# Performance work log

Hardware: AMD Instinct MI355X
Metric: run time of the kernel (lower is better)

## Reference

```python
import math
import jax, jax.numpy as jnp
import numpy as np

B, S, D_MODEL, H = 2, 2048, 1024, 16
D_HEAD = D_MODEL // H
NEG = -90000000000.0


def setup_inputs() -> dict:
    key = jax.random.key(0)
    ks = jax.random.split(key, 12)
    scale = 1.0 / math.sqrt(D_MODEL)
    return {
        "Q": jax.random.normal(ks[0], (B, S, D_MODEL), jnp.float32),
        "K": jax.random.normal(ks[1], (B, S, D_MODEL), jnp.float32),
        "V": jax.random.normal(ks[2], (B, S, D_MODEL), jnp.float32),
        "mask": jax.random.randint(ks[3], (B, 1, S, S), 0, 2).astype(bool),
        "Wq": jax.random.normal(ks[4], (D_MODEL, D_MODEL), jnp.float32) * scale,
        "bq": jnp.zeros((D_MODEL,), jnp.float32),
        "Wk": jax.random.normal(ks[5], (D_MODEL, D_MODEL), jnp.float32) * scale,
        "bk": jnp.zeros((D_MODEL,), jnp.float32),
        "Wv": jax.random.normal(ks[6], (D_MODEL, D_MODEL), jnp.float32) * scale,
        "bv": jnp.zeros((D_MODEL,), jnp.float32),
        "Wo": jax.random.normal(ks[7], (D_MODEL, D_MODEL), jnp.float32) * scale,
        "bo": jnp.zeros((D_MODEL,), jnp.float32),
    }


def _split_heads(x):
    # (B, S, D) -> (B, H, S, Dh)
    b, s, _ = x.shape
    return x.reshape(b, s, H, D_HEAD).transpose(0, 2, 1, 3)


def reference(Q, K, V, mask, Wq, bq, Wk, bk, Wv, bv, Wo, bo):
    q = _split_heads(Q @ Wq.T + bq)
    k = _split_heads(K @ Wk.T + bk)
    v = _split_heads(V @ Wv.T + bv)
    # scaled dot product with additive mask (mask.float() * -9e10)
    scores = jnp.einsum("bhqd,bhkd->bhqk", q, k) / math.sqrt(D_HEAD)
    scores = scores + mask.astype(scores.dtype) * NEG
    attn = jax.nn.softmax(scores, axis=-1)
    ctx = jnp.einsum("bhqk,bhkd->bhqd", attn, v)  # (B, H, S, Dh)
    ctx = ctx.transpose(0, 2, 1, 3).reshape(Q.shape[0], q.shape[2], D_MODEL)
    return ctx @ Wo.T + bo
```

## Files before the change

kernel.cpp:

```cpp
#include <hip/hip_runtime.h>
#include <hip/hip_bf16.h>


typedef __bf16 bf16x8 __attribute__((ext_vector_type(8)));
typedef __bf16 bf16x4 __attribute__((ext_vector_type(4)));
typedef float f32x4 __attribute__((ext_vector_type(4)));

#define S_LEN 2048
#define DM 1024
#define NH 16
#define DH 64
#define MROWS 4096

#define QSCALE 0.18033688011112042f

static __device__ __forceinline__ unsigned short f2bf(float f) {
    __bf16 b = (__bf16)f;
    unsigned short u; __builtin_memcpy(&u, &b, 2); return u;
}

static __device__ __forceinline__ float exp2_hw(float x) {
#if __has_builtin(__builtin_amdgcn_exp2f)
    return __builtin_amdgcn_exp2f(x);
#else
    float r; asm("v_exp_f32 %0, %1" : "=v"(r) : "v"(x)); return r;
#endif
}

static __device__ __forceinline__ bf16x8 cvt8(float4 a, float4 b) {
    bf16x8 o;
    o[0] = (__bf16)a.x; o[1] = (__bf16)a.y; o[2] = (__bf16)a.z; o[3] = (__bf16)a.w;
    o[4] = (__bf16)b.x; o[5] = (__bf16)b.y; o[6] = (__bf16)b.z; o[7] = (__bf16)b.w;
    return o;
}

__global__ __launch_bounds__(256)
void prep(const int* __restrict__ m, unsigned* __restrict__ mb,
          const float* __restrict__ Q, unsigned short* __restrict__ dQ,
          const float* __restrict__ K, unsigned short* __restrict__ dK,
          const float* __restrict__ V, unsigned short* __restrict__ dV,
          const float* __restrict__ W0, unsigned short* __restrict__ dW0,
          const float* __restrict__ W1, unsigned short* __restrict__ dW1,
          const float* __restrict__ W2, unsigned short* __restrict__ dW2,
          const float* __restrict__ W3, unsigned short* __restrict__ dW3)
{
    const int bx = blockIdx.x, tid = threadIdx.x;
    if (bx < 1024) {
        const int lane = tid & 63, w = tid >> 6;
        const int row = bx * 4 + w;
        const int* src = m + (size_t)row * S_LEN;
        unsigned* dst = mb + (size_t)row * (S_LEN / 32);
        for (int i = 0; i < 32; i++) {
            int v = src[i * 64 + lane];
            unsigned long long bm = __ballot(v != 0);
            if (lane == 0) { dst[i*2] = (unsigned)bm; dst[i*2+1] = (unsigned)(bm >> 32); }
        }
    } else if (bx < 7168) {
        int t = bx - 1024;
        int which = t >> 11;
        const float* s = which == 0 ? Q : which == 1 ? K : V;
        unsigned short* d = which == 0 ? dQ : which == 1 ? dK : dV;
        int i = ((t & 2047) * 256 + tid) * 8;
        float4 a = *(const float4*)(s + i);
        float4 b = *(const float4*)(s + i + 4);
        *(bf16x8*)(d + i) = cvt8(a, b);
    } else {
        int t = bx - 7168;
        int which = t >> 9;
        const float* s = which == 0 ? W0 : which == 1 ? W1 : which == 2 ? W2 : W3;
        unsigned short* d = which == 0 ? dW0 : which == 1 ? dW1 : which == 2 ? dW2 : dW3;
        int i = ((t & 511) * 256 + tid) * 8;
        float4 a = *(const float4*)(s + i);
        float4 b = *(const float4*)(s + i + 4);
        *(bf16x8*)(d + i) = cvt8(a, b);
    }
}

__global__ __launch_bounds__(256)
void gemm128(const unsigned short* __restrict__ X0, const unsigned short* __restrict__ X1,
             const unsigned short* __restrict__ X2,
             const unsigned short* __restrict__ W0, const unsigned short* __restrict__ W1,
             const unsigned short* __restrict__ W2,
             const float* __restrict__ b0, const float* __restrict__ b1,
             const float* __restrict__ b2,
             unsigned short* __restrict__ d0, unsigned short* __restrict__ d1,
             unsigned short* __restrict__ d2)
{
    __shared__ __align__(16) unsigned short As[128 * 32];
    __shared__ __align__(16) unsigned short Bs[128 * 32];

    const int bid = blockIdx.x + blockIdx.y * 8 + blockIdx.z * 256;
    const int xcd = bid & 7;
    const int t   = bid >> 3;
    const int z   = t >> 5;
    const int u   = t & 31;
    const int nt  = u & 7;
    const int mt  = xcd * 4 + (u >> 3);

    const unsigned short* X = z == 0 ? X0 : z == 1 ? X1 : X2;
    const unsigned short* W = z == 0 ? W0 : z == 1 ? W1 : W2;
    const float* bias        = z == 0 ? b0 : z == 1 ? b1 : b2;
    unsigned short* dstb     = z == 0 ? d0 : z == 1 ? d1 : d2;

    const int tid  = threadIdx.x;
    const int m0   = mt * 128;
    const int n0   = nt * 128;
    const int lane = tid & 63;
    const int w    = tid >> 6;
    const int wm   = (w >> 1) * 64, wn = (w & 1) * 64;
    const int lr   = lane & 15;
    const int lg   = lane >> 4;

    f32x4 acc[4][4];
#pragma unroll
    for (int i = 0; i < 4; i++)
#pragma unroll
        for (int j = 0; j < 4; j++) acc[i][j] = f32x4{0.f, 0.f, 0.f, 0.f};

    for (int k0 = 0; k0 < DM; k0 += 32) {
        __syncthreads();
#pragma unroll
        for (int j = 0; j < 2; j++) {
            int e = tid + j * 256;
            int row = e >> 2, c8 = (e & 3) * 8;
            __builtin_amdgcn_global_load_lds(
                (const __attribute__((address_space(1))) unsigned*)&X[(size_t)(m0 + row) * DM + k0 + c8],
                (__attribute__((address_space(3))) unsigned*)&As[e * 8], 16, 0, 0);
            __builtin_amdgcn_global_load_lds(
                (const __attribute__((address_space(1))) unsigned*)&W[(size_t)(n0 + row) * DM + k0 + c8],
                (__attribute__((address_space(3))) unsigned*)&Bs[e * 8], 16, 0, 0);
        }
        __syncthreads();
        bf16x8 af[4], bfr[4];
#pragma unroll
        for (int mi = 0; mi < 4; mi++)
            af[mi] = *(const bf16x8*)(&As[(wm + mi * 16 + lr) * 32 + lg * 8]);
#pragma unroll
        for (int ni = 0; ni < 4; ni++)
            bfr[ni] = *(const bf16x8*)(&Bs[(wn + ni * 16 + lr) * 32 + lg * 8]);
#pragma unroll
        for (int mi = 0; mi < 4; mi++)
#pragma unroll
            for (int ni = 0; ni < 4; ni++)
                acc[mi][ni] = __builtin_amdgcn_mfma_f32_16x16x32_bf16(
                    af[mi], bfr[ni], acc[mi][ni], 0, 0, 0);
    }

#pragma unroll
    for (int mi = 0; mi < 4; mi++) {
#pragma unroll
        for (int ni = 0; ni < 4; ni++) {
            const int gcol = n0 + wn + ni * 16 + lr;
            const float bv = bias[gcol];
            const int grow0 = m0 + wm + mi * 16 + lg * 4;
            if (z == 2) {
                int b = grow0 >> 11, s = grow0 & (S_LEN - 1);
                int h = gcol >> 6, dh = gcol & 63;
                bf16x4 pk;
#pragma unroll
                for (int r = 0; r < 4; r++) pk[r] = (__bf16)(acc[mi][ni][r] + bv);
                size_t di = ((size_t)(b * NH + h) * DH + dh) * S_LEN + s;
                *(bf16x4*)(&dstb[di]) = pk;
            } else {
#pragma unroll
                for (int r = 0; r < 4; r++) {
                    int grow = grow0 + r;
                    float v = acc[mi][ni][r] + bv;
                    if (z == 0) v *= QSCALE;
                    int b = grow >> 11, s = grow & (S_LEN - 1);
                    int h = gcol >> 6, dh = gcol & 63;
                    dstb[((size_t)(b * NH + h) * S_LEN + s) * DH + dh] = f2bf(v);
                }
            }
        }
    }
}

__global__ __launch_bounds__(256, 4)
void gemm_out(const unsigned short* __restrict__ X, const unsigned short* __restrict__ W,
              const float* __restrict__ bias, float* __restrict__ dst)
{
    __shared__ __align__(16) unsigned short As[128 * 32];
    __shared__ __align__(16) unsigned short Bs[64 * 32];

    const int bid = blockIdx.x + blockIdx.y * 16;
    const int xcd = bid & 7;
    const int u   = bid >> 3;
    const int nt  = u & 15;
    const int mt  = xcd * 4 + (u >> 4);

    const int tid  = threadIdx.x;
    const int m0   = mt * 128;
    const int n0   = nt * 64;
    const int lane = tid & 63;
    const int w    = tid >> 6;
    const int wm   = (w >> 1) * 64, wn = (w & 1) * 32;
    const int lr   = lane & 15;
    const int lg   = lane >> 4;

    f32x4 acc[4][2];
#pragma unroll
    for (int i = 0; i < 4; i++)
#pragma unroll
        for (int j = 0; j < 2; j++) acc[i][j] = f32x4{0.f, 0.f, 0.f, 0.f};

    for (int k0 = 0; k0 < DM; k0 += 32) {
        __syncthreads();
#pragma unroll
        for (int j = 0; j < 2; j++) {
            int e = tid + j * 256;
            int row = e >> 2, c8 = (e & 3) * 8;
            __builtin_amdgcn_global_load_lds(
                (const __attribute__((address_space(1))) unsigned*)&X[(size_t)(m0 + row) * DM + k0 + c8],
                (__attribute__((address_space(3))) unsigned*)&As[e * 8], 16, 0, 0);
        }
        {
            int row = tid >> 2, c8 = (tid & 3) * 8;
            __builtin_amdgcn_global_load_lds(
                (const __attribute__((address_space(1))) unsigned*)&W[(size_t)(n0 + row) * DM + k0 + c8],
                (__attribute__((address_space(3))) unsigned*)&Bs[tid * 8], 16, 0, 0);
        }
        __syncthreads();
        bf16x8 af[4], bfr[2];
#pragma unroll
        for (int mi = 0; mi < 4; mi++)
            af[mi] = *(const bf16x8*)(&As[(wm + mi * 16 + lr) * 32 + lg * 8]);
#pragma unroll
        for (int ni = 0; ni < 2; ni++)
            bfr[ni] = *(const bf16x8*)(&Bs[(wn + ni * 16 + lr) * 32 + lg * 8]);
#pragma unroll
        for (int mi = 0; mi < 4; mi++)
#pragma unroll
            for (int ni = 0; ni < 2; ni++)
                acc[mi][ni] = __builtin_amdgcn_mfma_f32_16x16x32_bf16(
                    af[mi], bfr[ni], acc[mi][ni], 0, 0, 0);
    }
#pragma unroll
    for (int mi = 0; mi < 4; mi++)
#pragma unroll
        for (int ni = 0; ni < 2; ni++) {
            const int gcol = n0 + wn + ni * 16 + lr;
            const float bv = bias[gcol];
            const int grow0 = m0 + wm + mi * 16 + lg * 4;
#pragma unroll
            for (int r = 0; r < 4; r++)
                dst[(size_t)(grow0 + r) * DM + gcol] = acc[mi][ni][r] + bv;
        }
}

__global__ __launch_bounds__(256, 3)
void attn(const unsigned short* __restrict__ q_ws,
          const unsigned short* __restrict__ k_ws,
          const unsigned short* __restrict__ vt_ws,
          const unsigned* __restrict__ mbits,
          unsigned short* __restrict__ ctx)
{
    __shared__ __align__(16) unsigned short Ks[2][64 * 72];
    __shared__ __align__(16) unsigned short Vs[2][64 * 72];
    __shared__ __align__(16) unsigned short Pq[4][16 * 72];
    const int tid = threadIdx.x, lane = tid & 63, w = tid >> 6;
    const int lr = lane & 15, lg = lane >> 4;

    const int i    = blockIdx.x;
    const int xcd  = i & 7;
    const int slot = i >> 3;
    const int bh   = xcd * 4 + (slot >> 4);
    const int qblk = slot & 15;
    const int b  = bh >> 4;
    const int h  = bh & 15;
    const int q0 = qblk * 128 + w * 32;
    const int qA = q0 + lr;
    const int qB = q0 + 16 + lr;

    const int srow = tid >> 3;
    const int sseg = tid & 7;

    const unsigned short* qh = q_ws + (size_t)bh * S_LEN * DH;
    const unsigned short* kh = k_ws + (size_t)bh * S_LEN * DH;
    const unsigned short* vh = vt_ws + (size_t)bh * DH * S_LEN;
    const unsigned* mrA = mbits + (size_t)(b * S_LEN + qA) * (S_LEN / 32);
    const unsigned* mrB = mbits + (size_t)(b * S_LEN + qB) * (S_LEN / 32);

    bf16x8 aqA[2], aqB[2];
#pragma unroll
    for (int c = 0; c < 2; c++) {
        aqA[c] = *(const bf16x8*)(&qh[(size_t)qA * DH + c * 32 + lg * 8]);
        aqB[c] = *(const bf16x8*)(&qh[(size_t)qB * DH + c * 32 + lg * 8]);
    }

    bf16x8 ones;
#pragma unroll
    for (int j = 0; j < 8; j++) ones[j] = (__bf16)1.0f;

    f32x4 accA[4], accB[4], accRA, accRB;
#pragma unroll
    for (int di = 0; di < 4; di++) {
        accA[di] = f32x4{0.f, 0.f, 0.f, 0.f};
        accB[di] = f32x4{0.f, 0.f, 0.f, 0.f};
    }
    accRA = f32x4{0.f, 0.f, 0.f, 0.f};
    accRB = f32x4{0.f, 0.f, 0.f, 0.f};

    uint4 kreg0, kreg1, vreg0, vreg1;
    kreg0 = *(const uint4*)(&kh[(size_t)(srow)      * DH + sseg * 8]);
    kreg1 = *(const uint4*)(&kh[(size_t)(srow + 32) * DH + sseg * 8]);
    vreg0 = *(const uint4*)(&vh[(size_t)(srow)      * S_LEN + sseg * 8]);
    vreg1 = *(const uint4*)(&vh[(size_t)(srow + 32) * S_LEN + sseg * 8]);
    *(uint4*)(&Ks[0][(srow)      * 72 + sseg * 8]) = kreg0;
    *(uint4*)(&Ks[0][(srow + 32) * 72 + sseg * 8]) = kreg1;
    *(uint4*)(&Vs[0][(srow)      * 72 + sseg * 8]) = vreg0;
    *(uint4*)(&Vs[0][(srow + 32) * 72 + sseg * 8]) = vreg1;
    kreg0 = *(const uint4*)(&kh[(size_t)(64 + srow)      * DH + sseg * 8]);
    kreg1 = *(const uint4*)(&kh[(size_t)(64 + srow + 32) * DH + sseg * 8]);
    vreg0 = *(const uint4*)(&vh[(size_t)(srow)      * S_LEN + 64 + sseg * 8]);
    vreg1 = *(const uint4*)(&vh[(size_t)(srow + 32) * S_LEN + 64 + sseg * 8]);
    __syncthreads();

    unsigned short* pq = &Pq[w][0];

    for (int it = 0; it < 32; it++) {
        const int cur = it & 1;
        const unsigned short* Kc = &Ks[cur][0];
        const unsigned short* Vc = &Vs[cur][0];
        if (it < 31) {
            unsigned short* Kn = &Ks[cur ^ 1][0];
            unsigned short* Vn = &Vs[cur ^ 1][0];
            *(uint4*)(&Kn[(srow)      * 72 + sseg * 8]) = kreg0;
            *(uint4*)(&Kn[(srow + 32) * 72 + sseg * 8]) = kreg1;
            *(uint4*)(&Vn[(srow)      * 72 + sseg * 8]) = vreg0;
            *(uint4*)(&Vn[(srow + 32) * 72 + sseg * 8]) = vreg1;
        }
        if (it < 30) {
            const int kn = (it + 2) * 64;
            kreg0 = *(const uint4*)(&kh[(size_t)(kn + srow)      * DH + sseg * 8]);
            kreg1 = *(const uint4*)(&kh[(size_t)(kn + srow + 32) * DH + sseg * 8]);
            vreg0 = *(const uint4*)(&vh[(size_t)(srow)      * S_LEN + kn + sseg * 8]);
            vreg1 = *(const uint4*)(&vh[(size_t)(srow + 32) * S_LEN + kn + sseg * 8]);
        }

        const uint2 mwA = *(const uint2*)(&mrA[it * 2]);
        const uint2 mwB = *(const uint2*)(&mrB[it * 2]);

        f32x4 sA[4], sB[4];
#pragma unroll
        for (int ni = 0; ni < 4; ni++) {
            bf16x8 ak0 = *(const bf16x8*)(&Kc[(ni * 16 + lr) * 72 + lg * 8]);
            bf16x8 ak1 = *(const bf16x8*)(&Kc[(ni * 16 + lr) * 72 + 32 + lg * 8]);
            f32x4 tA = __builtin_amdgcn_mfma_f32_16x16x32_bf16(ak0, aqA[0], f32x4{0.f,0.f,0.f,0.f}, 0,0,0);
            tA = __builtin_amdgcn_mfma_f32_16x16x32_bf16(ak1, aqA[1], tA, 0,0,0);
            f32x4 tB = __builtin_amdgcn_mfma_f32_16x16x32_bf16(ak0, aqB[0], f32x4{0.f,0.f,0.f,0.f}, 0,0,0);
            tB = __builtin_amdgcn_mfma_f32_16x16x32_bf16(ak1, aqB[1], tB, 0,0,0);
            sA[ni] = tA; sB[ni] = tB;
        }

#pragma unroll
        for (int ni = 0; ni < 4; ni++) {
            unsigned wA = (ni & 2) ? mwA.y : mwA.x;
            unsigned wB = (ni & 2) ? mwB.y : mwB.x;
            unsigned nibA = wA >> ((ni & 1) * 16 + lg * 4);
            unsigned nibB = wB >> ((ni & 1) * 16 + lg * 4);
#pragma unroll
            for (int r = 0; r < 4; r++) {
                float pA = exp2_hw(sA[ni][r]);
                float pB = exp2_hw(sB[ni][r]);
                sA[ni][r] = (nibA & (1u << r)) ? 0.f : pA;
                sB[ni][r] = (nibB & (1u << r)) ? 0.f : pB;
            }
        }

        bf16x8 av0[4], av1[4];
#pragma unroll
        for (int ni = 0; ni < 4; ni++) {
            bf16x4 pkA;
#pragma unroll
            for (int r = 0; r < 4; r++) pkA[r] = (__bf16)sA[ni][r];
            *(bf16x4*)(&pq[lr * 72 + ni * 16 + lg * 4]) = pkA;
        }
        bf16x8 bpA0 = *(const bf16x8*)(&pq[lr * 72 + lg * 8]);
        bf16x8 bpA1 = *(const bf16x8*)(&pq[lr * 72 + 32 + lg * 8]);
#pragma unroll
        for (int di = 0; di < 4; di++) {
            av0[di] = *(const bf16x8*)(&Vc[(di * 16 + lr) * 72 + lg * 8]);
            av1[di] = *(const bf16x8*)(&Vc[(di * 16 + lr) * 72 + 32 + lg * 8]);
            accA[di] = __builtin_amdgcn_mfma_f32_16x16x32_bf16(av0[di], bpA0, accA[di], 0, 0, 0);
            accA[di] = __builtin_amdgcn_mfma_f32_16x16x32_bf16(av1[di], bpA1, accA[di], 0, 0, 0);
        }
        accRA = __builtin_amdgcn_mfma_f32_16x16x32_bf16(ones, bpA0, accRA, 0, 0, 0);
        accRA = __builtin_amdgcn_mfma_f32_16x16x32_bf16(ones, bpA1, accRA, 0, 0, 0);

#pragma unroll
        for (int ni = 0; ni < 4; ni++) {
            bf16x4 pkB;
#pragma unroll
            for (int r = 0; r < 4; r++) pkB[r] = (__bf16)sB[ni][r];
            *(bf16x4*)(&pq[lr * 72 + ni * 16 + lg * 4]) = pkB;
        }
        bf16x8 bpB0 = *(const bf16x8*)(&pq[lr * 72 + lg * 8]);
        bf16x8 bpB1 = *(const bf16x8*)(&pq[lr * 72 + 32 + lg * 8]);
#pragma unroll
        for (int di = 0; di < 4; di++) {
            accB[di] = __builtin_amdgcn_mfma_f32_16x16x32_bf16(av0[di], bpB0, accB[di], 0, 0, 0);
            accB[di] = __builtin_amdgcn_mfma_f32_16x16x32_bf16(av1[di], bpB1, accB[di], 0, 0, 0);
        }
        accRB = __builtin_amdgcn_mfma_f32_16x16x32_bf16(ones, bpB0, accRB, 0, 0, 0);
        accRB = __builtin_amdgcn_mfma_f32_16x16x32_bf16(ones, bpB1, accRB, 0, 0, 0);

        __syncthreads();
    }

    const float invA = 1.0f / fmaxf(accRA[0], 1e-37f);
    const float invB = 1.0f / fmaxf(accRB[0], 1e-37f);

    unsigned short* crowA = &ctx[((size_t)(b * S_LEN + qA)) * DM + h * DH];
    unsigned short* crowB = &ctx[((size_t)(b * S_LEN + qB)) * DM + h * DH];
#pragma unroll
    for (int di = 0; di < 4; di++) {
        bf16x4 oA, oB;
#pragma unroll
        for (int r = 0; r < 4; r++) {
            oA[r] = (__bf16)(accA[di][r] * invA);
            oB[r] = (__bf16)(accB[di][r] * invB);
        }
        *(bf16x4*)(&crowA[di * 16 + lg * 4]) = oA;
        *(bf16x4*)(&crowB[di * 16 + lg * 4]) = oB;
    }
}

extern "C" void kernel_launch(void* const* d_in, const int* in_sizes, int n_in,
                              void* d_out, int out_size, void* d_ws, size_t ws_size,
                              hipStream_t stream)
{
    (void)in_sizes; (void)n_in; (void)out_size; (void)ws_size;
    const float* Q  = (const float*)d_in[0];
    const float* K  = (const float*)d_in[1];
    const float* V  = (const float*)d_in[2];
    const int*   Mk = (const int*)d_in[3];
    const float* Wq = (const float*)d_in[4];
    const float* bq = (const float*)d_in[5];
    const float* Wk = (const float*)d_in[6];
    const float* bk = (const float*)d_in[7];
    const float* Wv = (const float*)d_in[8];
    const float* bv = (const float*)d_in[9];
    const float* Wo = (const float*)d_in[10];
    const float* bo = (const float*)d_in[11];

    const int NX = MROWS * DM;
    const int NW = DM * DM;

    unsigned short* q_ws  = (unsigned short*)d_ws;
    unsigned short* k_ws  = q_ws + (size_t)NX;
    unsigned short* vt_ws = k_ws + (size_t)NX;
    unsigned short* ctx   = vt_ws + (size_t)NX;
    unsigned*       mbits = (unsigned*)(ctx + (size_t)NX);
    unsigned short* Wbq   = (unsigned short*)(mbits + (size_t)MROWS * (S_LEN / 32));
    unsigned short* Wbk   = Wbq + (size_t)NW;
    unsigned short* Wbv   = Wbk + (size_t)NW;
    unsigned short* Wbo   = Wbv + (size_t)NW;
    unsigned short* Xbq   = Wbo + (size_t)NW;
    unsigned short* Xbk   = Xbq + (size_t)NX;
    unsigned short* Xbv   = Xbk + (size_t)NX;
    float* out = (float*)d_out;

    dim3 blk(256);
    prep<<<dim3(9216), blk, 0, stream>>>(Mk, mbits, Q, Xbq, K, Xbk, V, Xbv,
                                         Wq, Wbq, Wk, Wbk, Wv, Wbv, Wo, Wbo);

    gemm128<<<dim3(8, 32, 3), blk, 0, stream>>>(Xbq, Xbk, Xbv, Wbq, Wbk, Wbv,
                                                bq, bk, bv, q_ws, k_ws, vt_ws);

    attn<<<dim3(512), blk, 0, stream>>>(q_ws, k_ws, vt_ws, mbits, ctx);

    gemm_out<<<dim3(16, 32), blk, 0, stream>>>(ctx, Wbo, bo, out);
}
```

Before: 265.0 us.

## Double-buffer GEMM LDS loads and move attention P transpose into registers via permlane

Both projection GEMMs now double-buffer their LDS tiles, so the next K-slice is issued through global_load_lds while MFMAs run on the current one, and each iteration needs one barrier instead of two. In the attention kernel, the P matrix is packed with v_cvt_pk_bf16_f32 and rearranged across lanes with permlane32/permlane16 swaps instead of a round trip through LDS. The Pq scratch buffer is removed and the PV MFMAs for both query groups are interleaved. s_setprio is raised around MFMA bursts, and launch bounds drop to 2 blocks per CU, which doubles LDS use and may reduce occupancy.

After: 261.4 us. About the same (-1.4%).

```diff
diff --git a/kernel.cpp b/kernel.cpp
--- a/kernel.cpp
+++ b/kernel.cpp
@@ -25,6 +25,18 @@
 #else
     float r; asm("v_exp_f32 %0, %1" : "=v"(r) : "v"(x)); return r;
 #endif
+}
+
+static __device__ __forceinline__ unsigned cvtpk_bf16(float lo, float hi) {
+    unsigned r;
+    asm("v_cvt_pk_bf16_f32 %0, %1, %2" : "=v"(r) : "v"(lo), "v"(hi));
+    return r;
+}
+static __device__ __forceinline__ void pl32swap(unsigned &x, unsigned &y) {
+    asm volatile("v_permlane32_swap_b32 %0, %1" : "+v"(x), "+v"(y));
+}
+static __device__ __forceinline__ void pl16swap(unsigned &x, unsigned &y) {
+    asm volatile("v_permlane16_swap_b32 %0, %1" : "+v"(x), "+v"(y));
 }
 
 static __device__ __forceinline__ bf16x8 cvt8(float4 a, float4 b) {
@@ -86,8 +98,8 @@
              unsigned short* __restrict__ d0, unsigned short* __restrict__ d1,
              unsigned short* __restrict__ d2)
 {
-    __shared__ __align__(16) unsigned short As[128 * 32];
-    __shared__ __align__(16) unsigned short Bs[128 * 32];
+    __shared__ __align__(16) unsigned short As[2][128 * 32];
+    __shared__ __align__(16) unsigned short Bs[2][128 * 32];
 
     const int bid = blockIdx.x + blockIdx.y * 8 + blockIdx.z * 256;
     const int xcd = bid & 7;
@@ -111,40 +123,54 @@
     const int lr   = lane & 15;
     const int lg   = lane >> 4;
 
+    const int srow = tid >> 2, sc8 = (tid & 3) * 8;
+    const int srow1 = (tid + 256) >> 2, sc81 = ((tid + 256) & 3) * 8;
+
     f32x4 acc[4][4];
 #pragma unroll
     for (int i = 0; i < 4; i++)
 #pragma unroll
         for (int j = 0; j < 4; j++) acc[i][j] = f32x4{0.f, 0.f, 0.f, 0.f};
 
+#define G128_STAGE(buf, kk)                                                          \
+    do {                                                                             \
+        __builtin_amdgcn_global_load_lds(                                            \
+            (const __attribute__((address_space(1))) unsigned*)&X[(size_t)(m0 + srow) * DM + (kk) + sc8],   \
+            (__attribute__((address_space(3))) unsigned*)&As[buf][tid * 8], 16, 0, 0);                      \
+        __builtin_amdgcn_global_load_lds(                                            \
+            (const __attribute__((address_space(1))) unsigned*)&W[(size_t)(n0 + srow) * DM + (kk) + sc8],   \
+            (__attribute__((address_space(3))) unsigned*)&Bs[buf][tid * 8], 16, 0, 0);                      \
+        __builtin_amdgcn_global_load_lds(                                            \
+            (const __attribute__((address_space(1))) unsigned*)&X[(size_t)(m0 + srow1) * DM + (kk) + sc81], \
+            (__attribute__((address_space(3))) unsigned*)&As[buf][(tid + 256) * 8], 16, 0, 0);              \
+        __builtin_amdgcn_global_load_lds(                                            \
+            (const __attribute__((address_space(1))) unsigned*)&W[(size_t)(n0 + srow1) * DM + (kk) + sc81], \
+            (__attribute__((address_space(3))) unsigned*)&Bs[buf][(tid + 256) * 8], 16, 0, 0);              \
+    } while (0)
+
+    G128_STAGE(0, 0);
+    __syncthreads();
+
     for (int k0 = 0; k0 < DM; k0 += 32) {
-        __syncthreads();
-#pragma unroll
-        for (int j = 0; j < 2; j++) {
-            int e = tid + j * 256;
-            int row = e >> 2, c8 = (e & 3) * 8;
-            __builtin_amdgcn_global_load_lds(
-                (const __attribute__((address_space(1))) unsigned*)&X[(size_t)(m0 + row) * DM + k0 + c8],
-                (__attribute__((address_space(3))) unsigned*)&As[e * 8], 16, 0, 0);
-            __builtin_amdgcn_global_load_lds(
-                (const __attribute__((address_space(1))) unsigned*)&W[(size_t)(n0 + row) * DM + k0 + c8],
-                (__attribute__((address_space(3))) unsigned*)&Bs[e * 8], 16, 0, 0);
-        }
-        __syncthreads();
+        const int cur = (k0 >> 5) & 1;
+        if (k0 + 32 < DM) G128_STAGE(cur ^ 1, k0 + 32);
+
         bf16x8 af[4], bfr[4];
 #pragma unroll
         for (int mi = 0; mi < 4; mi++)
-            af[mi] = *(const bf16x8*)(&As[(wm + mi * 16 + lr) * 32 + lg * 8]);
+            af[mi] = *(const bf16x8*)(&As[cur][(wm + mi * 16 + lr) * 32 + lg * 8]);
 #pragma unroll
         for (int ni = 0; ni < 4; ni++)
-            bfr[ni] = *(const bf16x8*)(&Bs[(wn + ni * 16 + lr) * 32 + lg * 8]);
+            bfr[ni] = *(const bf16x8*)(&Bs[cur][(wn + ni * 16 + lr) * 32 + lg * 8]);
 #pragma unroll
         for (int mi = 0; mi < 4; mi++)
 #pragma unroll
             for (int ni = 0; ni < 4; ni++)
                 acc[mi][ni] = __builtin_amdgcn_mfma_f32_16x16x32_bf16(
                     af[mi], bfr[ni], acc[mi][ni], 0, 0, 0);
-    }
+        __syncthreads();
+    }
+#undef G128_STAGE
 
 #pragma unroll
     for (int mi = 0; mi < 4; mi++) {
@@ -176,12 +202,12 @@
     }
 }
 
-__global__ __launch_bounds__(256, 4)
+__global__ __launch_bounds__(256, 2)
 void gemm_out(const unsigned short* __restrict__ X, const unsigned short* __restrict__ W,
               const float* __restrict__ bias, float* __restrict__ dst)
 {
-    __shared__ __align__(16) unsigned short As[128 * 32];
-    __shared__ __align__(16) unsigned short Bs[64 * 32];
+    __shared__ __align__(16) unsigned short As[2][128 * 32];
+    __shared__ __align__(16) unsigned short Bs[2][64 * 32];
 
     const int bid = blockIdx.x + blockIdx.y * 16;
     const int xcd = bid & 7;
@@ -198,43 +224,52 @@
     const int lr   = lane & 15;
     const int lg   = lane >> 4;
 
+    const int srow = tid >> 2, sc8 = (tid & 3) * 8;
+    const int srow1 = (tid + 256) >> 2, sc81 = ((tid + 256) & 3) * 8;
+
     f32x4 acc[4][2];
 #pragma unroll
     for (int i = 0; i < 4; i++)
 #pragma unroll
         for (int j = 0; j < 2; j++) acc[i][j] = f32x4{0.f, 0.f, 0.f, 0.f};
 
+#define GOUT_STAGE(buf, kk)                                                          \
+    do {                                                                             \
+        __builtin_amdgcn_global_load_lds(                                            \
+            (const __attribute__((address_space(1))) unsigned*)&X[(size_t)(m0 + srow) * DM + (kk) + sc8],   \
+            (__attribute__((address_space(3))) unsigned*)&As[buf][tid * 8], 16, 0, 0);                      \
+        __builtin_amdgcn_global_load_lds(                                            \
+            (const __attribute__((address_space(1))) unsigned*)&X[(size_t)(m0 + srow1) * DM + (kk) + sc81], \
+            (__attribute__((address_space(3))) unsigned*)&As[buf][(tid + 256) * 8], 16, 0, 0);              \
+        __builtin_amdgcn_global_load_lds(                                            \
+            (const __attribute__((address_space(1))) unsigned*)&W[(size_t)(n0 + srow) * DM + (kk) + sc8],   \
+            (__attribute__((address_space(3))) unsigned*)&Bs[buf][tid * 8], 16, 0, 0);                      \
+    } while (0)
+
+    GOUT_STAGE(0, 0);
+    __syncthreads();
+
     for (int k0 = 0; k0 < DM; k0 += 32) {
-        __syncthreads();
-#pragma unroll
-        for (int j = 0; j < 2; j++) {
-            int e = tid + j * 256;
-            int row = e >> 2, c8 = (e & 3) * 8;
-            __builtin_amdgcn_global_load_lds(
-                (const __attribute__((address_space(1))) unsigned*)&X[(size_t)(m0 + row) * DM + k0 + c8],
-                (__attribute__((address_space(3))) unsigned*)&As[e * 8], 16, 0, 0);
-        }
-        {
-            int row = tid >> 2, c8 = (tid & 3) * 8;
-            __builtin_amdgcn_global_load_lds(
-                (const __attribute__((address_space(1))) unsigned*)&W[(size_t)(n0 + row) * DM + k0 + c8],
-                (__attribute__((address_space(3))) unsigned*)&Bs[tid * 8], 16, 0, 0);
-        }
-        __syncthreads();
+        const int cur = (k0 >> 5) & 1;
+        if (k0 + 32 < DM) GOUT_STAGE(cur ^ 1, k0 + 32);
+
         bf16x8 af[4], bfr[2];
 #pragma unroll
         for (int mi = 0; mi < 4; mi++)
-            af[mi] = *(const bf16x8*)(&As[(wm + mi * 16 + lr) * 32 + lg * 8]);
+            af[mi] = *(const bf16x8*)(&As[cur][(wm + mi * 16 + lr) * 32 + lg * 8]);
 #pragma unroll
         for (int ni = 0; ni < 2; ni++)
-            bfr[ni] = *(const bf16x8*)(&Bs[(wn + ni * 16 + lr) * 32 + lg * 8]);
+            bfr[ni] = *(const bf16x8*)(&Bs[cur][(wn + ni * 16 + lr) * 32 + lg * 8]);
 #pragma unroll
         for (int mi = 0; mi < 4; mi++)
 #pragma unroll
             for (int ni = 0; ni < 2; ni++)
                 acc[mi][ni] = __builtin_amdgcn_mfma_f32_16x16x32_bf16(
                     af[mi], bfr[ni], acc[mi][ni], 0, 0, 0);
-    }
+        __syncthreads();
+    }
+#undef GOUT_STAGE
+
 #pragma unroll
     for (int mi = 0; mi < 4; mi++)
 #pragma unroll
@@ -248,7 +283,7 @@
         }
 }
 
-__global__ __launch_bounds__(256, 3)
+__global__ __launch_bounds__(256, 2)
 void attn(const unsigned short* __restrict__ q_ws,
           const unsigned short* __restrict__ k_ws,
           const unsigned short* __restrict__ vt_ws,
@@ -257,7 +292,6 @@
 {
     __shared__ __align__(16) unsigned short Ks[2][64 * 72];
     __shared__ __align__(16) unsigned short Vs[2][64 * 72];
-    __shared__ __align__(16) unsigned short Pq[4][16 * 72];
     const int tid = threadIdx.x, lane = tid & 63, w = tid >> 6;
     const int lr = lane & 15, lg = lane >> 4;
 
@@ -316,8 +350,6 @@
     vreg1 = *(const uint4*)(&vh[(size_t)(srow + 32) * S_LEN + 64 + sseg * 8]);
     __syncthreads();
 
-    unsigned short* pq = &Pq[w][0];
-
     for (int it = 0; it < 32; it++) {
         const int cur = it & 1;
         const unsigned short* Kc = &Ks[cur][0];
@@ -342,6 +374,7 @@
         const uint2 mwB = *(const uint2*)(&mrB[it * 2]);
 
         f32x4 sA[4], sB[4];
+        __builtin_amdgcn_s_setprio(1);
 #pragma unroll
         for (int ni = 0; ni < 4; ni++) {
             bf16x8 ak0 = *(const bf16x8*)(&Kc[(ni * 16 + lr) * 72 + lg * 8]);
@@ -352,6 +385,7 @@
             tB = __builtin_amdgcn_mfma_f32_16x16x32_bf16(ak1, aqB[1], tB, 0,0,0);
             sA[ni] = tA; sB[ni] = tB;
         }
+        __builtin_amdgcn_s_setprio(0);
 
 #pragma unroll
         for (int ni = 0; ni < 4; ni++) {
@@ -368,42 +402,46 @@
             }
         }
 
-        bf16x8 av0[4], av1[4];
+        unsigned wpA[8], wpB[8];
 #pragma unroll
         for (int ni = 0; ni < 4; ni++) {
-            bf16x4 pkA;
-#pragma unroll
-            for (int r = 0; r < 4; r++) pkA[r] = (__bf16)sA[ni][r];
-            *(bf16x4*)(&pq[lr * 72 + ni * 16 + lg * 4]) = pkA;
-        }
-        bf16x8 bpA0 = *(const bf16x8*)(&pq[lr * 72 + lg * 8]);
-        bf16x8 bpA1 = *(const bf16x8*)(&pq[lr * 72 + 32 + lg * 8]);
+            wpA[ni*2]   = cvtpk_bf16(sA[ni][0], sA[ni][1]);
+            wpA[ni*2+1] = cvtpk_bf16(sA[ni][2], sA[ni][3]);
+            wpB[ni*2]   = cvtpk_bf16(sB[ni][0], sB[ni][1]);
+            wpB[ni*2+1] = cvtpk_bf16(sB[ni][2], sB[ni][3]);
+        }
+#pragma unroll
+        for (int c = 0; c < 2; c++) {
+            pl32swap(wpA[c*4 + 0], wpA[c*4 + 2]);
+            pl32swap(wpA[c*4 + 1], wpA[c*4 + 3]);
+            pl16swap(wpA[c*4 + 0], wpA[c*4 + 2]);
+            pl16swap(wpA[c*4 + 1], wpA[c*4 + 3]);
+            pl32swap(wpB[c*4 + 0], wpB[c*4 + 2]);
+            pl32swap(wpB[c*4 + 1], wpB[c*4 + 3]);
+            pl16swap(wpB[c*4 + 0], wpB[c*4 + 2]);
+            pl16swap(wpB[c*4 + 1], wpB[c*4 + 3]);
+        }
+        bf16x8 bpA0, bpA1, bpB0, bpB1;
+        __builtin_memcpy(&bpA0, &wpA[0], 16);
+        __builtin_memcpy(&bpA1, &wpA[4], 16);
+        __builtin_memcpy(&bpB0, &wpB[0], 16);
+        __builtin_memcpy(&bpB1, &wpB[4], 16);
+
+        __builtin_amdgcn_s_setprio(1);
 #pragma unroll
         for (int di = 0; di < 4; di++) {
-            av0[di] = *(const bf16x8*)(&Vc[(di * 16 + lr) * 72 + lg * 8]);
-            av1[di] = *(const bf16x8*)(&Vc[(di * 16 + lr) * 72 + 32 + lg * 8]);
-            accA[di] = __builtin_amdgcn_mfma_f32_16x16x32_bf16(av0[di], bpA0, accA[di], 0, 0, 0);
-            accA[di] = __builtin_amdgcn_mfma_f32_16x16x32_bf16(av1[di], bpA1, accA[di], 0, 0, 0);
+            bf16x8 av0 = *(const bf16x8*)(&Vc[(di * 16 + lr) * 72 + lg * 8]);
+            bf16x8 av1 = *(const bf16x8*)(&Vc[(di * 16 + lr) * 72 + 32 + lg * 8]);
+            accA[di] = __builtin_amdgcn_mfma_f32_16x16x32_bf16(av0, bpA0, accA[di], 0, 0, 0);
+            accA[di] = __builtin_amdgcn_mfma_f32_16x16x32_bf16(av1, bpA1, accA[di], 0, 0, 0);
+            accB[di] = __builtin_amdgcn_mfma_f32_16x16x32_bf16(av0, bpB0, accB[di], 0, 0, 0);
+            accB[di] = __builtin_amdgcn_mfma_f32_16x16x32_bf16(av1, bpB1, accB[di], 0, 0, 0);
         }
         accRA = __builtin_amdgcn_mfma_f32_16x16x32_bf16(ones, bpA0, accRA, 0, 0, 0);
         accRA = __builtin_amdgcn_mfma_f32_16x16x32_bf16(ones, bpA1, accRA, 0, 0, 0);
-
-#pragma unroll
-        for (int ni = 0; ni < 4; ni++) {
-            bf16x4 pkB;
-#pragma unroll
-            for (int r = 0; r < 4; r++) pkB[r] = (__bf16)sB[ni][r];
-            *(bf16x4*)(&pq[lr * 72 + ni * 16 + lg * 4]) = pkB;
-        }
-        bf16x8 bpB0 = *(const bf16x8*)(&pq[lr * 72 + lg * 8]);
-        bf16x8 bpB1 = *(const bf16x8*)(&pq[lr * 72 + 32 + lg * 8]);
-#pragma unroll
-        for (int di = 0; di < 4; di++) {
-            accB[di] = __builtin_amdgcn_mfma_f32_16x16x32_bf16(av0[di], bpB0, accB[di], 0, 0, 0);
-            accB[di] = __builtin_amdgcn_mfma_f32_16x16x32_bf16(av1[di], bpB1, accB[di], 0, 0, 0);
-        }
         accRB = __builtin_amdgcn_mfma_f32_16x16x32_bf16(ones, bpB0, accRB, 0, 0, 0);
         accRB = __builtin_amdgcn_mfma_f32_16x16x32_bf16(ones, bpB1, accRB, 0, 0, 0);
+        __builtin_amdgcn_s_setprio(0);
 
         __syncthreads();
     }
```
